# Kernel tuning notes

Hardware: AMD Instinct MI355X
Metric: run time of the kernel (lower is better)

The kernel has to match this reference:

```python
import jax, jax.numpy as jnp
import numpy as np

INPUT_DIM = 128
OUTPUT_DIM = 64
EMBED_DIM = 3
B, S = 16, 2048
EPS = 1e-6


def setup_inputs() -> dict:
    key = jax.random.key(0)
    ks = jax.random.split(key, 8)
    scale = 0.05
    return {
        "x": jax.random.normal(ks[0], (B, S, INPUT_DIM), dtype=jnp.float32),
        "threshold": jnp.asarray(0.1, dtype=jnp.float32),
        "w1": jax.random.normal(ks[1], (INPUT_DIM, 2 * EMBED_DIM), dtype=jnp.float32) * scale,
        "b1": jnp.zeros((2 * EMBED_DIM,), dtype=jnp.float32),
        "w2": jax.random.normal(ks[2], (2 * EMBED_DIM, EMBED_DIM), dtype=jnp.float32) * scale,
        "b2": jnp.zeros((EMBED_DIM,), dtype=jnp.float32),
        "w3": jax.random.normal(ks[3], (4, OUTPUT_DIM), dtype=jnp.float32) * scale,
        "b3": jnp.zeros((OUTPUT_DIM,), dtype=jnp.float32),
    }


def reference(x, threshold, w1, b1, w2, b2, w3, b3):
    # phase-space embedding: Linear -> ReLU -> Linear   [B,S,E]
    h = jnp.maximum(x @ w1 + b1, 0.0) @ w2 + b2
    Bsz, Slen, _ = h.shape

    # pairwise euclidean distances (torch.cdist) per batch element [B,S,S]
    sq = jnp.sum(h * h, axis=-1)                         # [B,S]
    d2 = sq[:, :, None] + sq[:, None, :] - 2.0 * jnp.einsum('bse,bte->bst', h, h)
    dist = jnp.sqrt(jnp.maximum(d2, 0.0))

    # per-sample threshold = sigmoid(theta) * max(dist)
    thr = jax.nn.sigmoid(threshold) * jnp.max(dist, axis=(1, 2), keepdims=True)
    R = (dist < thr).astype(h.dtype)                     # recurrence matrix [B,S,S]

    total = jnp.sum(R, axis=(1, 2))                      # [B]
    rr = total / (Slen * Slen)                           # recurrence rate

    # sum of super-diagonals with offsets 1..min(S,10)-1
    idx = jnp.arange(Slen)
    off = idx[None, :] - idx[:, None]
    dmask = ((off >= 1) & (off <= min(Slen, 10) - 1)).astype(h.dtype)  # [S,S]
    diag_structures = jnp.einsum('bst,st->b', R, dmask)
    det = diag_structures / (total + EPS)

    # vertical structures: per column (over rows, axis=1), count runs of length >= 2.
    # a run of length>=2 starts at row i iff R[i]=1, R[i-1]=0 (or i=0), R[i+1]=1.
    prev = jnp.pad(R[:, :-1, :], ((0, 0), (1, 0), (0, 0)))
    nxt = jnp.pad(R[:, 1:, :], ((0, 0), (0, 1), (0, 0)))
    vert_structures = jnp.sum(R * (1.0 - prev) * nxt, axis=(1, 2))
    lam = vert_structures / (total + EPS)

    # 'entropy' term as written in the original (R is 0/1 valued)
    entr = -jnp.sum(R * jnp.log(R + EPS), axis=(1, 2))

    metrics = jnp.stack([rr, det, lam, entr], axis=-1)   # [B,4]
    return jnp.maximum(metrics @ w3 + b3, 0.0)           # [B,output_dim]
```

## Files before the change

kernel.cpp:

```cpp
#include <hip/hip_runtime.h>
#include <math.h>

#define B_ 16
#define S_ 2048
#define IN_DIM 128
#define E2 6
#define E_ 3
#define OUT_DIM 64


__global__ __launch_bounds__(256) void embed_kernel(
    const float* __restrict__ x, const float* __restrict__ w1,
    const float* __restrict__ b1, const float* __restrict__ w2,
    const float* __restrict__ b2, float* __restrict__ hws)
{
    int wave = threadIdx.x >> 6;
    int lane = threadIdx.x & 63;
#pragma unroll
    for (int rr = 0; rr < 4; ++rr) {
        int row = blockIdx.x * 16 + wave * 4 + rr;
        const float2* x2 = (const float2*)(x + (size_t)row * IN_DIM);
        float2 xv = x2[lane];
        const float* w1a = w1 + (2 * lane) * E2;
        float a[E2];
#pragma unroll
        for (int q = 0; q < E2; ++q)
            a[q] = xv.x * w1a[q] + xv.y * w1a[E2 + q];
#pragma unroll
        for (int q = 0; q < E2; ++q) {
#pragma unroll
            for (int off = 32; off >= 1; off >>= 1)
                a[q] += __shfl_xor(a[q], off, 64);
        }
        if (lane == 0) {
            float r[E2];
#pragma unroll
            for (int q = 0; q < E2; ++q) r[q] = fmaxf(a[q] + b1[q], 0.f);
            float h[E_];
#pragma unroll
            for (int e = 0; e < E_; ++e) {
                float s = b2[e];
#pragma unroll
                for (int q = 0; q < E2; ++q) s += r[q] * w2[q * E_ + e];
                h[e] = s;
            }
            float sq = h[0] * h[0] + h[1] * h[1] + h[2] * h[2];
            ((float4*)hws)[row] = make_float4(h[0], h[1], h[2], sq);
        }
    }
}

__global__ __launch_bounds__(256) void max_kernel(
    const float4* __restrict__ h4, float* __restrict__ pmax)
{
    int bid = blockIdx.x;
    int b  = bid >> 5;
    int rb = bid & 31;
    int r0 = rb * 64;
    const float4* hb = h4 + (size_t)b * S_;
    __shared__ float4 sh[64];
    if (threadIdx.x < 64) {
        float4 rv = hb[r0 + threadIdx.x];
        sh[threadIdx.x] = make_float4(-2.f * rv.x, -2.f * rv.y, -2.f * rv.z, rv.w);
    }
    float4 hj[8];
#pragma unroll
    for (int c = 0; c < 8; ++c) hj[c] = hb[c * 256 + threadIdx.x];
    __syncthreads();
    float mc[8];
#pragma unroll
    for (int c = 0; c < 8; ++c) mc[c] = -1e30f;
    float4 rv = sh[63];
#pragma unroll 4
    for (int k = 62; k >= 0; --k) {
        float4 nx = sh[k];
#pragma unroll
        for (int c = 0; c < 8; ++c) {
            float t = fmaf(hj[c].x, rv.x,
                      fmaf(hj[c].y, rv.y,
                      fmaf(hj[c].z, rv.z, rv.w)));
            mc[c] = fmaxf(mc[c], t);
        }
        rv = nx;
    }
#pragma unroll
    for (int c = 0; c < 8; ++c) {
        float t = fmaf(hj[c].x, rv.x,
                  fmaf(hj[c].y, rv.y,
                  fmaf(hj[c].z, rv.z, rv.w)));
        mc[c] = fmaxf(mc[c], t);
    }
    float m = -1e30f;
#pragma unroll
    for (int c = 0; c < 8; ++c) m = fmaxf(m, mc[c] + hj[c].w);
    m = fmaxf(m, 0.f);
#pragma unroll
    for (int off = 32; off >= 1; off >>= 1)
        m = fmaxf(m, __shfl_xor(m, off, 64));
    __shared__ float wmax[4];
    int lane = threadIdx.x & 63, wave = threadIdx.x >> 6;
    if (lane == 0) wmax[wave] = m;
    __syncthreads();
    if (threadIdx.x == 0) {
        float mm = fmaxf(fmaxf(wmax[0], wmax[1]), fmaxf(wmax[2], wmax[3]));
        pmax[bid] = mm;
    }
}

__global__ __launch_bounds__(256) void stats_kernel(
    const float4* __restrict__ h4, const float* __restrict__ theta,
    const float* __restrict__ pmax, int4* __restrict__ pstat)
{
    int bid = blockIdx.x;
    int b  = bid >> 5;
    int rb = bid & 31;
    int r0 = rb * 64;
    const float4* hb = h4 + (size_t)b * S_;
    __shared__ float4 sh[66];
    if (threadIdx.x < 66) {
        int r = r0 - 1 + threadIdx.x;
        r = r < 0 ? 0 : (r >= S_ ? S_ - 1 : r);
        float4 rv = hb[r];
        sh[threadIdx.x] = make_float4(-2.f * rv.x, -2.f * rv.y, -2.f * rv.z, rv.w);
    }
    float4 hj[8];
#pragma unroll
    for (int c = 0; c < 8; ++c) hj[c] = hb[c * 256 + threadIdx.x];
    __syncthreads();

    int lane = threadIdx.x & 63;
    float pm = pmax[b * 32 + (lane & 31)];
#pragma unroll
    for (int off = 16; off >= 1; off >>= 1)
        pm = fmaxf(pm, __shfl_xor(pm, off, 64));
    float maxd2 = pm;

    float sig   = 1.f / (1.f + expf(-theta[0]));
    float thr2  = sig * sig * maxd2;
    float thrc[8];
#pragma unroll
    for (int c = 0; c < 8; ++c) thrc[c] = thr2 - hj[c].w;

    unsigned mlo[8], mhi[8];
#pragma unroll
    for (int c = 0; c < 8; ++c) { mlo[c] = 0u; mhi[c] = 0u; }

    float4 rv = sh[64];
#pragma unroll 4
    for (int k = 63; k >= 32; --k) {
        float4 nx = sh[k];
#pragma unroll
        for (int c = 0; c < 8; ++c) {
            float t = fmaf(hj[c].x, rv.x,
                      fmaf(hj[c].y, rv.y,
                      fmaf(hj[c].z, rv.z, rv.w)));
            mhi[c] = mhi[c] * 2u + ((t < thrc[c]) ? 1u : 0u);
        }
        rv = nx;
    }
#pragma unroll 4
    for (int k = 31; k >= 0; --k) {
        float4 nx = sh[k];
#pragma unroll
        for (int c = 0; c < 8; ++c) {
            float t = fmaf(hj[c].x, rv.x,
                      fmaf(hj[c].y, rv.y,
                      fmaf(hj[c].z, rv.z, rv.w)));
            mlo[c] = mlo[c] * 2u + ((t < thrc[c]) ? 1u : 0u);
        }
        rv = nx;
    }
    float4 pr = rv;
    float4 nxr = sh[65];

    int total = 0, diag = 0, vert = 0;
#pragma unroll
    for (int c = 0; c < 8; ++c) {
        int j = c * 256 + threadIdx.x;
        unsigned long long m = ((unsigned long long)mhi[c] << 32) | mlo[c];
        total += __popcll(m);
        float tp = fmaf(hj[c].x, pr.x, fmaf(hj[c].y, pr.y, fmaf(hj[c].z, pr.z, pr.w)));
        float tn = fmaf(hj[c].x, nxr.x, fmaf(hj[c].y, nxr.y, fmaf(hj[c].z, nxr.z, nxr.w)));
        unsigned long long prevbit = (r0 > 0) ? ((tp < thrc[c]) ? 1ull : 0ull) : 0ull;
        unsigned long long nextbit = (r0 + 64 < S_) ? ((tn < thrc[c]) ? 1ull : 0ull) : 0ull;
        unsigned long long notprev = ~((m << 1) | prevbit);
        vert += __popcll(m & notprev & ((m >> 1) | (nextbit << 63)));
        int lo = j - 9 - r0, hi = j - 1 - r0;
        if (hi >= 0 && lo <= 63) {
            int l = lo < 0 ? 0 : lo;
            int h = hi > 63 ? 63 : hi;
            unsigned long long bandm = ((1ull << (h - l + 1)) - 1ull) << l;
            diag += __popcll(m & bandm);
        }
    }

    int dv = (diag << 16) | vert;
#pragma unroll
    for (int off = 32; off >= 1; off >>= 1) {
        total += __shfl_xor(total, off, 64);
        dv    += __shfl_xor(dv,    off, 64);
    }
    __shared__ int wsum[4][2];
    int wave = threadIdx.x >> 6;
    if (lane == 0) { wsum[wave][0] = total; wsum[wave][1] = dv; }
    __syncthreads();
    if (threadIdx.x == 0) {
        int t = 0, d = 0, v = 0;
#pragma unroll
        for (int w = 0; w < 4; ++w) {
            t += wsum[w][0];
            d += wsum[w][1] >> 16;
            v += wsum[w][1] & 0xFFFF;
        }
        pstat[bid] = make_int4(t, d, v, 0);
    }
}

__global__ __launch_bounds__(256) void finalize_kernel(
    const int4* __restrict__ pstat,
    const float* __restrict__ w3, const float* __restrict__ b3,
    float* __restrict__ out)
{
    __shared__ float stot[16], sdia[16], sver[16];
    int tid = threadIdx.x;
    if (tid < 16) {
        int t = 0, d = 0, v = 0;
        for (int i = 0; i < 32; ++i) {
            int4 p = pstat[tid * 32 + i];
            t += p.x; d += p.y; v += p.z;
        }
        stot[tid] = (float)t; sdia[tid] = (float)d; sver[tid] = (float)v;
    }
    __syncthreads();
#pragma unroll
    for (int q = 0; q < 4; ++q) {
        int idx = q * 256 + tid;
        int b = idx >> 6, o = idx & 63;
        float total = stot[b], diag = sdia[b], vert = sver[b];
        float rr  = total / (float)(S_ * S_);
        float det = diag / (total + 1e-6f);
        float lam = vert / (total + 1e-6f);
        float entr = -total * logf(1.0f + 1e-6f);
        float r = b3[o] + rr  * w3[0 * OUT_DIM + o]
                        + det * w3[1 * OUT_DIM + o]
                        + lam * w3[2 * OUT_DIM + o]
                        + entr * w3[3 * OUT_DIM + o];
        out[idx] = fmaxf(r, 0.f);
    }
}

extern "C" void kernel_launch(void* const* d_in, const int* in_sizes, int n_in,
                              void* d_out, int out_size, void* d_ws, size_t ws_size,
                              hipStream_t stream) {
    const float* x     = (const float*)d_in[0];
    const float* theta = (const float*)d_in[1];
    const float* w1    = (const float*)d_in[2];
    const float* b1    = (const float*)d_in[3];
    const float* w2    = (const float*)d_in[4];
    const float* b2    = (const float*)d_in[5];
    const float* w3    = (const float*)d_in[6];
    const float* b3    = (const float*)d_in[7];
    float* out = (float*)d_out;
    float* hws = (float*)d_ws;
    float* pmax = (float*)((char*)d_ws + 524288);
    int4*  pstat = (int4*)((char*)d_ws + 526336);

    hipLaunchKernelGGL(embed_kernel, dim3(B_ * S_ / 16), dim3(256), 0, stream,
                       x, w1, b1, w2, b2, hws);
    hipLaunchKernelGGL(max_kernel, dim3(B_ * 32), dim3(256), 0, stream,
                       (const float4*)hws, pmax);
    hipLaunchKernelGGL(stats_kernel, dim3(B_ * 32), dim3(256), 0, stream,
                       (const float4*)hws, theta, pmax, pstat);
    hipLaunchKernelGGL(finalize_kernel, dim3(1), dim3(256), 0, stream,
                       pstat, w3, b3, out);
}
```

Measured before the change: 110.8 us.

## Exploit distance symmetry in max pass and fuse finalize into stats via last-block counter

```diff
diff --git a/kernel.cpp b/kernel.cpp
--- a/kernel.cpp
+++ b/kernel.cpp
@@ -12,8 +12,10 @@
 __global__ __launch_bounds__(256) void embed_kernel(
     const float* __restrict__ x, const float* __restrict__ w1,
     const float* __restrict__ b1, const float* __restrict__ w2,
-    const float* __restrict__ b2, float* __restrict__ hws)
-{
+    const float* __restrict__ b2, float* __restrict__ hws,
+    int* __restrict__ done)
+{
+    if (blockIdx.x == 0 && threadIdx.x == 0) *done = 0;
     int wave = threadIdx.x >> 6;
     int lane = threadIdx.x & 63;
 #pragma unroll
@@ -48,6 +50,42 @@
             ((float4*)hws)[row] = make_float4(h[0], h[1], h[2], sq);
         }
     }
+}
+
+template<int CMIN>
+__device__ __forceinline__ float max_tile(const float4* __restrict__ hb,
+                                          const float4* sh, int tid)
+{
+    float4 hj[8 - CMIN];
+#pragma unroll
+    for (int c = 0; c < 8 - CMIN; ++c) hj[c] = hb[(c + CMIN) * 256 + tid];
+    float mc[8 - CMIN];
+#pragma unroll
+    for (int c = 0; c < 8 - CMIN; ++c) mc[c] = -1e30f;
+    float4 rv = sh[63];
+#pragma unroll 4
+    for (int k = 62; k >= 0; --k) {
+        float4 nx = sh[k];
+#pragma unroll
+        for (int c = 0; c < 8 - CMIN; ++c) {
+            float t = fmaf(hj[c].x, rv.x,
+                      fmaf(hj[c].y, rv.y,
+                      fmaf(hj[c].z, rv.z, rv.w)));
+            mc[c] = fmaxf(mc[c], t);
+        }
+        rv = nx;
+    }
+#pragma unroll
+    for (int c = 0; c < 8 - CMIN; ++c) {
+        float t = fmaf(hj[c].x, rv.x,
+                  fmaf(hj[c].y, rv.y,
+                  fmaf(hj[c].z, rv.z, rv.w)));
+        mc[c] = fmaxf(mc[c], t);
+    }
+    float m = -1e30f;
+#pragma unroll
+    for (int c = 0; c < 8 - CMIN; ++c) m = fmaxf(m, mc[c] + hj[c].w);
+    return m;
 }
 
 __global__ __launch_bounds__(256) void max_kernel(
@@ -63,36 +101,9 @@
         float4 rv = hb[r0 + threadIdx.x];
         sh[threadIdx.x] = make_float4(-2.f * rv.x, -2.f * rv.y, -2.f * rv.z, rv.w);
     }
-    float4 hj[8];
-#pragma unroll
-    for (int c = 0; c < 8; ++c) hj[c] = hb[c * 256 + threadIdx.x];
-    __syncthreads();
-    float mc[8];
-#pragma unroll
-    for (int c = 0; c < 8; ++c) mc[c] = -1e30f;
-    float4 rv = sh[63];
-#pragma unroll 4
-    for (int k = 62; k >= 0; --k) {
-        float4 nx = sh[k];
-#pragma unroll
-        for (int c = 0; c < 8; ++c) {
-            float t = fmaf(hj[c].x, rv.x,
-                      fmaf(hj[c].y, rv.y,
-                      fmaf(hj[c].z, rv.z, rv.w)));
-            mc[c] = fmaxf(mc[c], t);
-        }
-        rv = nx;
-    }
-#pragma unroll
-    for (int c = 0; c < 8; ++c) {
-        float t = fmaf(hj[c].x, rv.x,
-                  fmaf(hj[c].y, rv.y,
-                  fmaf(hj[c].z, rv.z, rv.w)));
-        mc[c] = fmaxf(mc[c], t);
-    }
-    float m = -1e30f;
-#pragma unroll
-    for (int c = 0; c < 8; ++c) m = fmaxf(m, mc[c] + hj[c].w);
+    __syncthreads();
+    float m = (rb < 16) ? max_tile<0>(hb, sh, threadIdx.x)
+                        : max_tile<4>(hb, sh, threadIdx.x);
     m = fmaxf(m, 0.f);
 #pragma unroll
     for (int off = 32; off >= 1; off >>= 1)
@@ -109,7 +120,10 @@
 
 __global__ __launch_bounds__(256) void stats_kernel(
     const float4* __restrict__ h4, const float* __restrict__ theta,
-    const float* __restrict__ pmax, int4* __restrict__ pstat)
+    const float* __restrict__ pmax, int4* __restrict__ pstat,
+    int* __restrict__ done,
+    const float* __restrict__ w3, const float* __restrict__ b3,
+    float* __restrict__ out)
 {
     int bid = blockIdx.x;
     int b  = bid >> 5;
@@ -154,7 +168,7 @@
             float t = fmaf(hj[c].x, rv.x,
                       fmaf(hj[c].y, rv.y,
                       fmaf(hj[c].z, rv.z, rv.w)));
-            mhi[c] = mhi[c] * 2u + ((t < thrc[c]) ? 1u : 0u);
+            mhi[c] = mhi[c] + mhi[c] + ((t < thrc[c]) ? 1u : 0u);
         }
         rv = nx;
     }
@@ -166,7 +180,7 @@
             float t = fmaf(hj[c].x, rv.x,
                       fmaf(hj[c].y, rv.y,
                       fmaf(hj[c].z, rv.z, rv.w)));
-            mlo[c] = mlo[c] * 2u + ((t < thrc[c]) ? 1u : 0u);
+            mlo[c] = mlo[c] + mlo[c] + ((t < thrc[c]) ? 1u : 0u);
         }
         rv = nx;
     }
@@ -204,6 +218,7 @@
     int wave = threadIdx.x >> 6;
     if (lane == 0) { wsum[wave][0] = total; wsum[wave][1] = dv; }
     __syncthreads();
+    __shared__ int slast;
     if (threadIdx.x == 0) {
         int t = 0, d = 0, v = 0;
 #pragma unroll
@@ -213,39 +228,41 @@
             v += wsum[w][1] & 0xFFFF;
         }
         pstat[bid] = make_int4(t, d, v, 0);
-    }
-}
-
-__global__ __launch_bounds__(256) void finalize_kernel(
-    const int4* __restrict__ pstat,
-    const float* __restrict__ w3, const float* __restrict__ b3,
-    float* __restrict__ out)
-{
-    __shared__ float stot[16], sdia[16], sver[16];
-    int tid = threadIdx.x;
-    if (tid < 16) {
-        int t = 0, d = 0, v = 0;
-        for (int i = 0; i < 32; ++i) {
-            int4 p = pstat[tid * 32 + i];
-            t += p.x; d += p.y; v += p.z;
-        }
-        stot[tid] = (float)t; sdia[tid] = (float)d; sver[tid] = (float)v;
-    }
-    __syncthreads();
-#pragma unroll
-    for (int q = 0; q < 4; ++q) {
-        int idx = q * 256 + tid;
-        int b = idx >> 6, o = idx & 63;
-        float total = stot[b], diag = sdia[b], vert = sver[b];
-        float rr  = total / (float)(S_ * S_);
-        float det = diag / (total + 1e-6f);
-        float lam = vert / (total + 1e-6f);
-        float entr = -total * logf(1.0f + 1e-6f);
-        float r = b3[o] + rr  * w3[0 * OUT_DIM + o]
-                        + det * w3[1 * OUT_DIM + o]
-                        + lam * w3[2 * OUT_DIM + o]
-                        + entr * w3[3 * OUT_DIM + o];
-        out[idx] = fmaxf(r, 0.f);
+        __threadfence();
+        int prev = atomicAdd(done, 1);
+        slast = (prev == 511) ? 1 : 0;
+    }
+    __syncthreads();
+    if (slast) {
+        __shared__ float stot[16], sdia[16], sver[16];
+        int tid = threadIdx.x;
+        if (tid < 16) {
+            int t = 0, d = 0, v = 0;
+            const int* ps = (const int*)pstat;
+            for (int i = 0; i < 32; ++i) {
+                int base = (tid * 32 + i) * 4;
+                t += __hip_atomic_load(&ps[base + 0], __ATOMIC_RELAXED, __HIP_MEMORY_SCOPE_AGENT);
+                d += __hip_atomic_load(&ps[base + 1], __ATOMIC_RELAXED, __HIP_MEMORY_SCOPE_AGENT);
+                v += __hip_atomic_load(&ps[base + 2], __ATOMIC_RELAXED, __HIP_MEMORY_SCOPE_AGENT);
+            }
+            stot[tid] = (float)t; sdia[tid] = (float)d; sver[tid] = (float)v;
+        }
+        __syncthreads();
+#pragma unroll
+        for (int q = 0; q < 4; ++q) {
+            int idx = q * 256 + tid;
+            int ob = idx >> 6, o = idx & 63;
+            float tt = stot[ob], dd = sdia[ob], vv = sver[ob];
+            float rr2  = tt / (float)(S_ * S_);
+            float det  = dd / (tt + 1e-6f);
+            float lam  = vv / (tt + 1e-6f);
+            float entr = -tt * logf(1.0f + 1e-6f);
+            float r = b3[o] + rr2 * w3[0 * OUT_DIM + o]
+                            + det * w3[1 * OUT_DIM + o]
+                            + lam * w3[2 * OUT_DIM + o]
+                            + entr * w3[3 * OUT_DIM + o];
+            out[idx] = fmaxf(r, 0.f);
+        }
     }
 }
 
@@ -264,13 +281,12 @@
     float* hws = (float*)d_ws;
     float* pmax = (float*)((char*)d_ws + 524288);
     int4*  pstat = (int4*)((char*)d_ws + 526336);
+    int*   done  = (int*)((char*)d_ws + 534528);
 
     hipLaunchKernelGGL(embed_kernel, dim3(B_ * S_ / 16), dim3(256), 0, stream,
-                       x, w1, b1, w2, b2, hws);
+                       x, w1, b1, w2, b2, hws, done);
     hipLaunchKernelGGL(max_kernel, dim3(B_ * 32), dim3(256), 0, stream,
                        (const float4*)hws, pmax);
     hipLaunchKernelGGL(stats_kernel, dim3(B_ * 32), dim3(256), 0, stream,
-                       (const float4*)hws, theta, pmax, pstat);
-    hipLaunchKernelGGL(finalize_kernel, dim3(1), dim3(256), 0, stream,
-                       pstat, w3, b3, out);
-}
+                       (const float4*)hws, theta, pmax, pstat, done, w3, b3, out);
+}
```

Measured after the change: 116.4 us. 5.1% more time.

## Fuse max, stats and finalize into one kernel with per-batch spin barrier

Applied to the files above, without the earlier changes.

```diff
diff --git a/kernel.cpp b/kernel.cpp
--- a/kernel.cpp
+++ b/kernel.cpp
@@ -12,13 +12,15 @@
 __global__ __launch_bounds__(256) void embed_kernel(
     const float* __restrict__ x, const float* __restrict__ w1,
     const float* __restrict__ b1, const float* __restrict__ w2,
-    const float* __restrict__ b2, float* __restrict__ hws)
+    const float* __restrict__ b2, float* __restrict__ hws,
+    int* __restrict__ cnt )
 {
+    if (blockIdx.x == 0 && threadIdx.x < 17) cnt[threadIdx.x] = 0;
     int wave = threadIdx.x >> 6;
     int lane = threadIdx.x & 63;
-#pragma unroll
-    for (int rr = 0; rr < 4; ++rr) {
-        int row = blockIdx.x * 16 + wave * 4 + rr;
+#pragma unroll 4
+    for (int rr = 0; rr < 16; ++rr) {
+        int row = blockIdx.x * 64 + wave * 16 + rr;
         const float2* x2 = (const float2*)(x + (size_t)row * IN_DIM);
         float2 xv = x2[lane];
         const float* w1a = w1 + (2 * lane) * E2;
@@ -50,66 +52,12 @@
     }
 }
 
-__global__ __launch_bounds__(256) void max_kernel(
-    const float4* __restrict__ h4, float* __restrict__ pmax)
-{
-    int bid = blockIdx.x;
-    int b  = bid >> 5;
-    int rb = bid & 31;
-    int r0 = rb * 64;
-    const float4* hb = h4 + (size_t)b * S_;
-    __shared__ float4 sh[64];
-    if (threadIdx.x < 64) {
-        float4 rv = hb[r0 + threadIdx.x];
-        sh[threadIdx.x] = make_float4(-2.f * rv.x, -2.f * rv.y, -2.f * rv.z, rv.w);
-    }
-    float4 hj[8];
-#pragma unroll
-    for (int c = 0; c < 8; ++c) hj[c] = hb[c * 256 + threadIdx.x];
-    __syncthreads();
-    float mc[8];
-#pragma unroll
-    for (int c = 0; c < 8; ++c) mc[c] = -1e30f;
-    float4 rv = sh[63];
-#pragma unroll 4
-    for (int k = 62; k >= 0; --k) {
-        float4 nx = sh[k];
-#pragma unroll
-        for (int c = 0; c < 8; ++c) {
-            float t = fmaf(hj[c].x, rv.x,
-                      fmaf(hj[c].y, rv.y,
-                      fmaf(hj[c].z, rv.z, rv.w)));
-            mc[c] = fmaxf(mc[c], t);
-        }
-        rv = nx;
-    }
-#pragma unroll
-    for (int c = 0; c < 8; ++c) {
-        float t = fmaf(hj[c].x, rv.x,
-                  fmaf(hj[c].y, rv.y,
-                  fmaf(hj[c].z, rv.z, rv.w)));
-        mc[c] = fmaxf(mc[c], t);
-    }
-    float m = -1e30f;
-#pragma unroll
-    for (int c = 0; c < 8; ++c) m = fmaxf(m, mc[c] + hj[c].w);
-    m = fmaxf(m, 0.f);
-#pragma unroll
-    for (int off = 32; off >= 1; off >>= 1)
-        m = fmaxf(m, __shfl_xor(m, off, 64));
-    __shared__ float wmax[4];
-    int lane = threadIdx.x & 63, wave = threadIdx.x >> 6;
-    if (lane == 0) wmax[wave] = m;
-    __syncthreads();
-    if (threadIdx.x == 0) {
-        float mm = fmaxf(fmaxf(wmax[0], wmax[1]), fmaxf(wmax[2], wmax[3]));
-        pmax[bid] = mm;
-    }
-}
-
-__global__ __launch_bounds__(256) void stats_kernel(
+__global__ __launch_bounds__(256) void rqa_kernel(
     const float4* __restrict__ h4, const float* __restrict__ theta,
-    const float* __restrict__ pmax, int4* __restrict__ pstat)
+    float* __restrict__ pmax, unsigned long long* __restrict__ pstat,
+    int* __restrict__ cnt, int* __restrict__ done,
+    const float* __restrict__ w3, const float* __restrict__ b3,
+    float* __restrict__ out)
 {
     int bid = blockIdx.x;
     int b  = bid >> 5;
@@ -117,6 +65,9 @@
     int r0 = rb * 64;
     const float4* hb = h4 + (size_t)b * S_;
     __shared__ float4 sh[66];
+    __shared__ float wmax[4];
+    __shared__ int wsum[4][2];
+    __shared__ int slast;
     if (threadIdx.x < 66) {
         int r = r0 - 1 + threadIdx.x;
         r = r < 0 ? 0 : (r >= S_ ? S_ - 1 : r);
@@ -127,9 +78,53 @@
 #pragma unroll
     for (int c = 0; c < 8; ++c) hj[c] = hb[c * 256 + threadIdx.x];
     __syncthreads();
-
-    int lane = threadIdx.x & 63;
-    float pm = pmax[b * 32 + (lane & 31)];
+    int lane = threadIdx.x & 63, wave = threadIdx.x >> 6;
+
+    float mc[8];
+#pragma unroll
+    for (int c = 0; c < 8; ++c) mc[c] = -1e30f;
+    {
+        float4 rv = sh[64];
+#pragma unroll 4
+        for (int k = 63; k >= 1; --k) {
+            float4 nx = sh[k];
+#pragma unroll
+            for (int c = 0; c < 8; ++c) {
+                float t = fmaf(hj[c].x, rv.x,
+                          fmaf(hj[c].y, rv.y,
+                          fmaf(hj[c].z, rv.z, rv.w)));
+                mc[c] = fmaxf(mc[c], t);
+            }
+            rv = nx;
+        }
+#pragma unroll
+        for (int c = 0; c < 8; ++c) {
+            float t = fmaf(hj[c].x, rv.x,
+                      fmaf(hj[c].y, rv.y,
+                      fmaf(hj[c].z, rv.z, rv.w)));
+            mc[c] = fmaxf(mc[c], t);
+        }
+    }
+    float m = -1e30f;
+#pragma unroll
+    for (int c = 0; c < 8; ++c) m = fmaxf(m, mc[c] + hj[c].w);
+    m = fmaxf(m, 0.f);
+#pragma unroll
+    for (int off = 32; off >= 1; off >>= 1)
+        m = fmaxf(m, __shfl_xor(m, off, 64));
+    if (lane == 0) wmax[wave] = m;
+    __syncthreads();
+    if (threadIdx.x == 0) {
+        float mm = fmaxf(fmaxf(wmax[0], wmax[1]), fmaxf(wmax[2], wmax[3]));
+        __hip_atomic_store(&pmax[bid], mm, __ATOMIC_RELEASE, __HIP_MEMORY_SCOPE_AGENT);
+        __hip_atomic_fetch_add(&cnt[b], 1, __ATOMIC_ACQ_REL, __HIP_MEMORY_SCOPE_AGENT);
+        while (__hip_atomic_load(&cnt[b], __ATOMIC_ACQUIRE, __HIP_MEMORY_SCOPE_AGENT) < 32)
+            __builtin_amdgcn_s_sleep(8);
+    }
+    __syncthreads();
+
+    float pm = __hip_atomic_load(&pmax[b * 32 + (lane & 31)],
+                                 __ATOMIC_RELAXED, __HIP_MEMORY_SCOPE_AGENT);
 #pragma unroll
     for (int off = 16; off >= 1; off >>= 1)
         pm = fmaxf(pm, __shfl_xor(pm, off, 64));
@@ -144,7 +139,6 @@
     unsigned mlo[8], mhi[8];
 #pragma unroll
     for (int c = 0; c < 8; ++c) { mlo[c] = 0u; mhi[c] = 0u; }
-
     float4 rv = sh[64];
 #pragma unroll 4
     for (int k = 63; k >= 32; --k) {
@@ -177,31 +171,28 @@
 #pragma unroll
     for (int c = 0; c < 8; ++c) {
         int j = c * 256 + threadIdx.x;
-        unsigned long long m = ((unsigned long long)mhi[c] << 32) | mlo[c];
-        total += __popcll(m);
+        unsigned long long mm = ((unsigned long long)mhi[c] << 32) | mlo[c];
+        total += __popcll(mm);
         float tp = fmaf(hj[c].x, pr.x, fmaf(hj[c].y, pr.y, fmaf(hj[c].z, pr.z, pr.w)));
         float tn = fmaf(hj[c].x, nxr.x, fmaf(hj[c].y, nxr.y, fmaf(hj[c].z, nxr.z, nxr.w)));
         unsigned long long prevbit = (r0 > 0) ? ((tp < thrc[c]) ? 1ull : 0ull) : 0ull;
         unsigned long long nextbit = (r0 + 64 < S_) ? ((tn < thrc[c]) ? 1ull : 0ull) : 0ull;
-        unsigned long long notprev = ~((m << 1) | prevbit);
-        vert += __popcll(m & notprev & ((m >> 1) | (nextbit << 63)));
+        unsigned long long notprev = ~((mm << 1) | prevbit);
+        vert += __popcll(mm & notprev & ((mm >> 1) | (nextbit << 63)));
         int lo = j - 9 - r0, hi = j - 1 - r0;
         if (hi >= 0 && lo <= 63) {
             int l = lo < 0 ? 0 : lo;
             int h = hi > 63 ? 63 : hi;
             unsigned long long bandm = ((1ull << (h - l + 1)) - 1ull) << l;
-            diag += __popcll(m & bandm);
-        }
-    }
-
+            diag += __popcll(mm & bandm);
+        }
+    }
     int dv = (diag << 16) | vert;
 #pragma unroll
     for (int off = 32; off >= 1; off >>= 1) {
         total += __shfl_xor(total, off, 64);
         dv    += __shfl_xor(dv,    off, 64);
     }
-    __shared__ int wsum[4][2];
-    int wave = threadIdx.x >> 6;
     if (lane == 0) { wsum[wave][0] = total; wsum[wave][1] = dv; }
     __syncthreads();
     if (threadIdx.x == 0) {
@@ -212,40 +203,43 @@
             d += wsum[w][1] >> 16;
             v += wsum[w][1] & 0xFFFF;
         }
-        pstat[bid] = make_int4(t, d, v, 0);
-    }
-}
-
-__global__ __launch_bounds__(256) void finalize_kernel(
-    const int4* __restrict__ pstat,
-    const float* __restrict__ w3, const float* __restrict__ b3,
-    float* __restrict__ out)
-{
-    __shared__ float stot[16], sdia[16], sver[16];
-    int tid = threadIdx.x;
-    if (tid < 16) {
-        int t = 0, d = 0, v = 0;
-        for (int i = 0; i < 32; ++i) {
-            int4 p = pstat[tid * 32 + i];
-            t += p.x; d += p.y; v += p.z;
-        }
-        stot[tid] = (float)t; sdia[tid] = (float)d; sver[tid] = (float)v;
-    }
-    __syncthreads();
-#pragma unroll
-    for (int q = 0; q < 4; ++q) {
-        int idx = q * 256 + tid;
-        int b = idx >> 6, o = idx & 63;
-        float total = stot[b], diag = sdia[b], vert = sver[b];
-        float rr  = total / (float)(S_ * S_);
-        float det = diag / (total + 1e-6f);
-        float lam = vert / (total + 1e-6f);
-        float entr = -total * logf(1.0f + 1e-6f);
-        float r = b3[o] + rr  * w3[0 * OUT_DIM + o]
-                        + det * w3[1 * OUT_DIM + o]
-                        + lam * w3[2 * OUT_DIM + o]
-                        + entr * w3[3 * OUT_DIM + o];
-        out[idx] = fmaxf(r, 0.f);
+        unsigned long long pk = ((unsigned long long)(unsigned)((d << 16) | v) << 32)
+                              | (unsigned long long)(unsigned)t;
+        __hip_atomic_store(&pstat[bid], pk, __ATOMIC_RELEASE, __HIP_MEMORY_SCOPE_AGENT);
+        int prev = __hip_atomic_fetch_add(done, 1, __ATOMIC_ACQ_REL, __HIP_MEMORY_SCOPE_AGENT);
+        slast = (prev == 511) ? 1 : 0;
+    }
+    __syncthreads();
+
+    if (slast) {
+        __shared__ int stot[16], sdia[16], sver[16];
+        int tid = threadIdx.x;
+        if (tid < 16) { stot[tid] = 0; sdia[tid] = 0; sver[tid] = 0; }
+        __syncthreads();
+        for (int i = tid; i < 512; i += 256) {
+            unsigned long long p = __hip_atomic_load(&pstat[i], __ATOMIC_RELAXED,
+                                                     __HIP_MEMORY_SCOPE_AGENT);
+            int bb = i >> 5;
+            atomicAdd(&stot[bb], (int)(p & 0xFFFFFFFFull));
+            atomicAdd(&sdia[bb], (int)(p >> 48));
+            atomicAdd(&sver[bb], (int)((p >> 32) & 0xFFFFull));
+        }
+        __syncthreads();
+#pragma unroll
+        for (int q = 0; q < 4; ++q) {
+            int idx = q * 256 + tid;
+            int ob = idx >> 6, o = idx & 63;
+            float tt = (float)stot[ob], dd = (float)sdia[ob], vv = (float)sver[ob];
+            float rr2  = tt / (float)(S_ * S_);
+            float det  = dd / (tt + 1e-6f);
+            float lam  = vv / (tt + 1e-6f);
+            float entr = -tt * logf(1.0f + 1e-6f);
+            float r = b3[o] + rr2 * w3[0 * OUT_DIM + o]
+                            + det * w3[1 * OUT_DIM + o]
+                            + lam * w3[2 * OUT_DIM + o]
+                            + entr * w3[3 * OUT_DIM + o];
+            out[idx] = fmaxf(r, 0.f);
+        }
     }
 }
 
@@ -263,14 +257,12 @@
     float* out = (float*)d_out;
     float* hws = (float*)d_ws;
     float* pmax = (float*)((char*)d_ws + 524288);
-    int4*  pstat = (int4*)((char*)d_ws + 526336);
-
-    hipLaunchKernelGGL(embed_kernel, dim3(B_ * S_ / 16), dim3(256), 0, stream,
-                       x, w1, b1, w2, b2, hws);
-    hipLaunchKernelGGL(max_kernel, dim3(B_ * 32), dim3(256), 0, stream,
-                       (const float4*)hws, pmax);
-    hipLaunchKernelGGL(stats_kernel, dim3(B_ * 32), dim3(256), 0, stream,
-                       (const float4*)hws, theta, pmax, pstat);
-    hipLaunchKernelGGL(finalize_kernel, dim3(1), dim3(256), 0, stream,
-                       pstat, w3, b3, out);
+    unsigned long long* pstat = (unsigned long long*)((char*)d_ws + 526336);
+    int*   cnt  = (int*)((char*)d_ws + 530432);
+    int*   done = cnt + 16;
+
+    hipLaunchKernelGGL(embed_kernel, dim3(B_ * S_ / 64), dim3(256), 0, stream,
+                       x, w1, b1, w2, b2, hws, cnt);
+    hipLaunchKernelGGL(rqa_kernel, dim3(B_ * 32), dim3(256), 0, stream,
+                       (const float4*)hws, theta, pmax, pstat, cnt, done, w3, b3, out);
 }
```

Result: slower. 132.8 us (+19.9%).
